# Kernel optimization log

Measured on AMD Instinct MI355X. Metric: run time of the kernel, lower is better.

Reference implementation:

```python
import jax, jax.numpy as jnp
import numpy as np

B, T = 64, 512
V, F, H = 30000, 256, 256
K = 32          # type_num
PAD, START, END = 0, 30, 31


def make_transition():
    # replicate the exact init order of the torch code
    t = jnp.zeros((K, K), jnp.float32)
    t = t.at[:, START].set(-10000.0)
    t = t.at[END, :].set(-10000.0)
    t = t.at[:, PAD].set(-10000.0)
    t = t.at[PAD, PAD].set(0.0)
    t = t.at[PAD, :END].set(0.0)
    return t


def setup_inputs() -> dict:
    key = jax.random.key(0)
    ks = jax.random.split(key, 12)
    x = jax.random.randint(ks[0], (B, T), 0, V, dtype=jnp.int32)
    tags = jax.random.randint(ks[1], (B, T), 1, START, dtype=jnp.int32)  # real tags, no pad/start/end
    lengths = jax.random.randint(ks[2], (B,), T // 2, T + 1, dtype=jnp.int32)
    mask = (jnp.arange(T, dtype=jnp.int32)[None, :] < lengths[:, None]).astype(jnp.int32)
    s = 0.05
    emb = jax.random.normal(ks[3], (V, F), jnp.float32) * (2.0 / (V + F)) ** 0.5 * 10  # xavier-ish
    w_ih_f = jax.random.normal(ks[4], (4 * H, F), jnp.float32) * s
    w_hh_f = jax.random.normal(ks[5], (4 * H, H), jnp.float32) * s
    b_f = jax.random.normal(ks[6], (4 * H,), jnp.float32) * s  # = b_ih + b_hh (they only ever sum)
    w_ih_b = jax.random.normal(ks[7], (4 * H, F), jnp.float32) * s
    w_hh_b = jax.random.normal(ks[8], (4 * H, H), jnp.float32) * s
    b_b = jax.random.normal(ks[9], (4 * H,), jnp.float32) * s
    w_fc = jax.random.normal(ks[10], (K, 2 * H), jnp.float32) * s
    b_fc = jax.random.normal(ks[11], (K,), jnp.float32) * s
    transition = make_transition()
    return dict(x=x, tags=tags, mask=mask, emb=emb,
                w_ih_f=w_ih_f, w_hh_f=w_hh_f, b_f=b_f,
                w_ih_b=w_ih_b, w_hh_b=w_hh_b, b_b=b_b,
                w_fc=w_fc, b_fc=b_fc, transition=transition)


def _lstm_scan(gx, w_hh):
    # gx: [T, B, 4H] precomputed input gates; PyTorch gate order i, f, g, o
    h0 = jnp.zeros((gx.shape[1], w_hh.shape[1]), gx.dtype)

    def step(carry, g):
        h, c = carry
        z = g + h @ w_hh.T
        i, f, gg, o = jnp.split(z, 4, axis=-1)
        c = jax.nn.sigmoid(f) * c + jax.nn.sigmoid(i) * jnp.tanh(gg)
        h = jax.nn.sigmoid(o) * jnp.tanh(c)
        return (h, c), h

    _, hs = jax.lax.scan(step, (h0, h0), gx)
    return hs  # [T, B, H]


def _crf_loss(scores, tags, mask, transition):
    # scores: [B, T, K], tags/mask: [B, T]
    maskf = mask.astype(scores.dtype)
    b_idx = jnp.arange(scores.shape[0])

    # ---- true path score ----
    first = transition[START, tags[:, 0]] + scores[b_idx, 0, tags[:, 0]]
    tag_sc = jnp.take_along_axis(scores, tags[..., None].astype(jnp.int32), axis=2)[..., 0]  # [B,T]
    tran_sc = transition[tags[:, :-1], tags[:, 1:]]  # [B,T-1]
    body = jnp.sum((tran_sc + tag_sc[:, 1:]) * maskf[:, 1:], axis=1)
    last_idx = jnp.sum(mask, axis=1) - 1
    last_tag = jnp.take_along_axis(tags, last_idx[:, None], axis=1)[:, 0]
    true_prob = first + body + transition[last_tag, END]

    # ---- partition (forward algorithm) via scan ----
    alpha0 = transition[START][None, :] + scores[:, 0]  # [B,K]

    def step(alpha, inp):
        sc, m = inp  # sc: [B,K], m: [B]
        new = jax.nn.logsumexp(alpha[:, :, None] + transition[None, :, :] + sc[:, None, :], axis=1)
        alpha = jnp.where(m[:, None] > 0, new, alpha)
        return alpha, None

    alpha, _ = jax.lax.scan(step, alpha0,
                            (scores.transpose(1, 0, 2)[1:], mask.T[1:]))
    total_prob = jax.nn.logsumexp(alpha + transition[:, END][None, :], axis=1)
    return -jnp.sum(true_prob - total_prob)


def reference(x, tags, mask, emb, w_ih_f, w_hh_f, b_f, w_ih_b, w_hh_b, b_b, w_fc, b_fc, transition):
    e = emb[x]                       # [B,T,F] embedding lookup (dropout = identity, eval mode)
    xt = e.transpose(1, 0, 2)        # [T,B,F]
    # forward direction
    h_f = _lstm_scan(xt @ w_ih_f.T + b_f, w_hh_f)           # [T,B,H]
    # backward direction: reverse time, scan, reverse back
    h_b = _lstm_scan((xt @ w_ih_b.T + b_b)[::-1], w_hh_b)[::-1]
    h = jnp.concatenate([h_f, h_b], axis=-1).transpose(1, 0, 2)  # [B,T,2H]
    scores = h @ w_fc.T + b_fc       # [B,T,K]
    return _crf_loss(scores, tags, mask, transition)
```

## Files before the change

### kernel.cpp

```cpp
#include <hip/hip_runtime.h>

typedef __attribute__((ext_vector_type(8))) short short8;
typedef __attribute__((ext_vector_type(4))) float floatx4;
typedef __attribute__((ext_vector_type(8))) int int8v;

__device__ __forceinline__ float bf2f(unsigned short u) {
    union { unsigned int i; float f; } c; c.i = ((unsigned int)u) << 16; return c.f;
}
__device__ __forceinline__ unsigned short f2bf(float f) {
    union { float f; unsigned int i; } c; c.f = f;
    unsigned int u = c.i;
    return (unsigned short)((u + 0x7FFFu + ((u >> 16) & 1u)) >> 16);
}
__device__ __forceinline__ unsigned short f2bf_rz(float f) {
    union { float f; unsigned int i; } c; c.f = f;
    return (unsigned short)(c.i >> 16);
}
__device__ __forceinline__ float sigm(float x) {
    return __builtin_amdgcn_rcpf(1.f + __expf(-x));
}
__device__ __forceinline__ float tanh_(float x) {
    return 1.f - 2.f * __builtin_amdgcn_rcpf(1.f + __expf(2.f * x));
}

__device__ __forceinline__ void glds16(const void* g, void* l) {
    __builtin_amdgcn_global_load_lds((const __attribute__((address_space(1))) unsigned int*)g,
                                     (__attribute__((address_space(3))) unsigned int*)l, 16, 0, 0);
}

__global__ void k_prep(const int* __restrict__ x, const float* __restrict__ emb,
                       unsigned short* __restrict__ et,
                       const float* __restrict__ wihf, const float* __restrict__ wihb,
                       const float* __restrict__ wfc, unsigned short* __restrict__ wbf,
                       const float* __restrict__ whhf, const float* __restrict__ whhb,
                       unsigned char* __restrict__ w8) {
    const int bid = blockIdx.x;
    if (bid < 4096) {
        int id = bid * 256 + threadIdx.x;
        int m = id >> 5, fi = (id & 31) << 3;
        int b = m & 63, t = m >> 6;
        int v = x[b * 512 + t];
        const float4* s = (const float4*)(emb + ((size_t)v << 8) + fi);
        float4 a = s[0], q = s[1];
        uint4 o;
        o.x = (unsigned)f2bf(a.x) | ((unsigned)f2bf(a.y) << 16);
        o.y = (unsigned)f2bf(a.z) | ((unsigned)f2bf(a.w) << 16);
        o.z = (unsigned)f2bf(q.x) | ((unsigned)f2bf(q.y) << 16);
        o.w = (unsigned)f2bf(q.z) | ((unsigned)f2bf(q.w) << 16);
        *(uint4*)(et + ((size_t)m << 8) + fi) = o;
    } else if (bid < 6176) {
        int i = (bid - 4096) * 256 + threadIdx.x;
        if (i >= 532480) return;
        float v;
        if (i < 262144) v = wihf[i];
        else if (i < 524288) v = wihb[i - 262144];
        else v = wfc[i - 524288];
        wbf[i] = f2bf(v);
    } else {
        int i = (bid - 6176) * 256 + threadIdx.x;
        if (i >= 262144) return;
        int e = i * 2;
        float a = (e < 262144) ? whhf[e] : whhb[e - 262144];
        float b = (e + 1 < 262144) ? whhf[e + 1] : whhb[e + 1 - 262144];
        int p = __builtin_amdgcn_cvt_pk_fp8_f32(a, b, 0, false);
        *(unsigned short*)(w8 + e) = (unsigned short)(p & 0xffff);
    }
}

__global__ __launch_bounds__(256, 2) void k_gx(const unsigned short* __restrict__ et,
                                               const unsigned short* __restrict__ wcat,
                                               const float* __restrict__ bfv, const float* __restrict__ bbv,
                                               unsigned short* __restrict__ gx) {
    __shared__ unsigned short As[4096];
    __shared__ unsigned short Bs[4096];
    const int tid = threadIdx.x;
    const int w = tid >> 6, l = tid & 63, quad = l >> 4, col = l & 15;
    const size_t m0 = (size_t)blockIdx.x * 128, n0 = (size_t)blockIdx.y * 128;
    floatx4 C[4][4];
    #pragma unroll
    for (int i = 0; i < 4; ++i)
        #pragma unroll
        for (int j = 0; j < 4; ++j) C[i][j] = (floatx4){0.f, 0.f, 0.f, 0.f};
    const int srow = tid >> 2, scol = (tid & 3) * 16;
    for (int it = 0; it < 8; ++it) {
        const char* ga = (const char*)et + (m0 + srow) * 512 + it * 64 + scol;
        const char* gb = (const char*)wcat + (n0 + srow) * 512 + it * 64 + scol;
        glds16(ga,             (char*)As + w * 1024);
        glds16(ga + 64 * 512,  (char*)As + 4096 + w * 1024);
        glds16(gb,             (char*)Bs + w * 1024);
        glds16(gb + 64 * 512,  (char*)Bs + 4096 + w * 1024);
        __syncthreads();
        short8 Af[4], Bf[4];
        #pragma unroll
        for (int i = 0; i < 4; ++i) {
            Af[i] = *(const short8*)(As + (((w & 1) * 64 + i * 16 + col) * 32 + quad * 8));
            Bf[i] = *(const short8*)(Bs + (((w >> 1) * 64 + i * 16 + col) * 32 + quad * 8));
        }
        #pragma unroll
        for (int i = 0; i < 4; ++i)
            #pragma unroll
            for (int j = 0; j < 4; ++j)
                C[i][j] = __builtin_amdgcn_mfma_f32_16x16x32_bf16(Af[i], Bf[j], C[i][j], 0, 0, 0);
        __syncthreads();
    }
    const int mw = (w & 1) * 64, nw = (w >> 1) * 64;
    #pragma unroll
    for (int j = 0; j < 4; ++j) {
        int n = (int)n0 + nw + j * 16 + col;
        float bias = (n < 1024) ? bfv[n] : bbv[n - 1024];
        size_t dbase = (size_t)(n >> 10) * 33554432 + (size_t)(n & 1023);
        #pragma unroll
        for (int i = 0; i < 4; ++i)
            #pragma unroll
            for (int r = 0; r < 4; ++r) {
                size_t m = m0 + mw + i * 16 + quad * 4 + r;
                gx[dbase + m * 1024] = f2bf(C[i][j][r] + bias);
            }
    }
}

__global__ __launch_bounds__(512, 2) void k_lstm(const unsigned char* __restrict__ w8_all,
                                                 const unsigned short* __restrict__ gx_all,
                                                 unsigned short* __restrict__ hcat) {
    const int d = blockIdx.x >> 5, bg = blockIdx.x & 31;
    const int tid = threadIdx.x, w = tid >> 6, l = tid & 63, quad = l >> 4, col = l & 15;
    const unsigned char* W = w8_all + (size_t)d * 262144;
    const unsigned short* G = gx_all + (size_t)d * 33554432;
    __shared__ __align__(16) unsigned char hld[2][2][288];

    int8v Wb[4][2][2];
    #pragma unroll
    for (int g = 0; g < 4; ++g)
        #pragma unroll
        for (int nt = 0; nt < 2; ++nt)
            #pragma unroll
            for (int kt = 0; kt < 2; ++kt)
                Wb[g][nt][kt] = *(const int8v*)(W + (size_t)(256 * g + 32 * w + 16 * nt + col) * 256
                                                + kt * 128 + quad * 32);
    for (int i = tid; i < 288; i += 512) ((unsigned int*)hld)[i] = 0;

    const int b = l >> 5, u = 32 * w + (l & 31);
    const int bglob = 2 * bg + b;
    const int nts = quad & 1;
    const int hsel = (l >> 3) & 1;
    float cst = 0.f;
    const long gstep = d ? -65536 : 65536;
    const long hstep = d ? -32768 : 32768;
    const unsigned short* gp = G + ((size_t)((d ? 511 : 0) * 64 + bglob) * 1024 + u);
    unsigned short* hp = hcat + ((size_t)((d ? 511 : 0) * 64 + bglob) * 512 + d * 256 + u);
    unsigned short gq0 = gp[0], gq1 = gp[256], gq2 = gp[512], gq3 = gp[768];
    gp += gstep;
    __syncthreads();

    #pragma clang loop unroll(disable)
    for (int step = 0; step < 512; ++step) {
        const int cur = step & 1;
        int8v Af[2];
        #pragma unroll
        for (int kt = 0; kt < 2; ++kt)
            Af[kt] = *(const int8v*)(&hld[cur][hsel][kt * 128 + quad * 32]);
        float z[4];
        #pragma unroll
        for (int g = 0; g < 4; ++g) {
            floatx4 c0 = (floatx4){0.f, 0.f, 0.f, 0.f};
            floatx4 c1 = (floatx4){0.f, 0.f, 0.f, 0.f};
            #pragma unroll
            for (int kt = 0; kt < 2; ++kt) {
                c0 = __builtin_amdgcn_mfma_scale_f32_16x16x128_f8f6f4(
                    Af[kt], Wb[g][0][kt], c0, 0, 0, 0, 0x7f7f7f7f, 0, 0x7f7f7f7f);
                c1 = __builtin_amdgcn_mfma_scale_f32_16x16x128_f8f6f4(
                    Af[kt], Wb[g][1][kt], c1, 0, 0, 0, 0x7f7f7f7f, 0, 0x7f7f7f7f);
            }
            z[g] = nts ? c1[0] : c0[0];
        }
        float vi = z[0] + bf2f(gq0);
        float vf = z[1] + bf2f(gq1);
        float vg = z[2] + bf2f(gq2);
        float vo = z[3] + bf2f(gq3);
        gq0 = gp[0]; gq1 = gp[256]; gq2 = gp[512]; gq3 = gp[768];
        gp += gstep;
        float cc = sigm(vf) * cst + sigm(vi) * tanh_(vg);
        cst = cc;
        float hf = sigm(vo) * tanh_(cc);
        *hp = f2bf_rz(hf);
        hp += hstep;
        int pk = __builtin_amdgcn_cvt_pk_fp8_f32(hf, hf, 0, false);
        hld[cur ^ 1][b][u] = (unsigned char)(pk & 0xff);
        __builtin_amdgcn_sched_barrier(0);
        asm volatile("s_waitcnt lgkmcnt(0)");
        __builtin_amdgcn_sched_barrier(0);
        __builtin_amdgcn_s_barrier();
        __builtin_amdgcn_sched_barrier(0);
    }
}

__global__ __launch_bounds__(256, 4) void k_scores(const unsigned short* __restrict__ hcat,
                                                   const unsigned short* __restrict__ wfc,
                                                   const float* __restrict__ bfc,
                                                   float* __restrict__ sc) {
    const int tid = threadIdx.x, w = tid >> 6, l = tid & 63, quad = l >> 4, col = l & 15;
    const int m0 = blockIdx.x * 64 + w * 16;
    floatx4 C0 = (floatx4){0.f, 0.f, 0.f, 0.f}, C1 = C0;
    #pragma unroll
    for (int kt = 0; kt < 16; ++kt) {
        short8 A  = *(const short8*)(hcat + (size_t)(m0 + col) * 512 + kt * 32 + quad * 8);
        short8 B0 = *(const short8*)(wfc + (size_t)col * 512 + kt * 32 + quad * 8);
        short8 B1 = *(const short8*)(wfc + (size_t)(16 + col) * 512 + kt * 32 + quad * 8);
        C0 = __builtin_amdgcn_mfma_f32_16x16x32_bf16(A, B0, C0, 0, 0, 0);
        C1 = __builtin_amdgcn_mfma_f32_16x16x32_bf16(A, B1, C1, 0, 0, 0);
    }
    float b0 = bfc[col], b1 = bfc[16 + col];
    #pragma unroll
    for (int r = 0; r < 4; ++r) {
        int m = m0 + quad * 4 + r;
        sc[(size_t)m * 32 + col] = C0[r] + b0;
        sc[(size_t)m * 32 + 16 + col] = C1[r] + b1;
    }
}

__global__ __launch_bounds__(1024, 1) void k_crf(const float* __restrict__ sc, const int* __restrict__ tags,
                                                 const int* __restrict__ mask, const float* __restrict__ tr,
                                                 float* __restrict__ out) {
    __shared__ float Tm[32][33];
    __shared__ float al[2][32];
    __shared__ float trueb;
    const int b = blockIdx.x, tid = threadIdx.x;
    { int i = tid >> 5, j = tid & 31; Tm[i][j] = tr[tid]; }
    __syncthreads();
    if (tid < 64) {
        float acc = 0.f; int cnt = 0;
        for (int t = tid; t < 512; t += 64) cnt += mask[b * 512 + t];
        for (int t = tid + 1; t < 512; t += 64) {
            if (mask[b * 512 + t]) {
                int tg = tags[b * 512 + t], tp = tags[b * 512 + t - 1];
                acc += Tm[tp][tg] + sc[((size_t)t * 64 + b) * 32 + tg];
            }
        }
        #pragma unroll
        for (int m = 1; m < 64; m <<= 1) { acc += __shfl_xor(acc, m); cnt += __shfl_xor(cnt, m); }
        if (tid == 0) {
            int tg0 = tags[b * 512];
            float first = Tm[30][tg0] + sc[(size_t)b * 32 + tg0];
            int lt = tags[b * 512 + cnt - 1];
            trueb = first + acc + Tm[lt][31];
        }
    }
    if (tid < 32) al[0][tid] = Tm[30][tid] + sc[(size_t)b * 32 + tid];
    __syncthreads();
    const int j = tid >> 5, i = tid & 31;
    int cur = 0;
    float scn = sc[((size_t)64 + b) * 32 + j];
    int mkn = mask[b * 512 + 1];
    #pragma clang loop unroll(disable)
    for (int t = 1; t < 512; ++t) {
        float v = al[cur][i] + Tm[i][j];
        float mx = v;
        #pragma unroll
        for (int m = 1; m < 32; m <<= 1) mx = fmaxf(mx, __shfl_xor(mx, m));
        float e = __expf(v - mx);
        #pragma unroll
        for (int m = 1; m < 32; m <<= 1) e += __shfl_xor(e, m);
        float nv = mx + __logf(e) + scn;
        int mk = mkn;
        int tn = t < 511 ? t + 1 : 511;
        scn = sc[((size_t)tn * 64 + b) * 32 + j];
        mkn = mask[b * 512 + tn];
        if (i == 0) al[cur ^ 1][j] = mk ? nv : al[cur][j];
        __syncthreads();
        cur ^= 1;
    }
    if (tid < 32) {
        float v = al[cur][tid] + Tm[tid][31];
        float mx = v;
        #pragma unroll
        for (int m = 1; m < 32; m <<= 1) mx = fmaxf(mx, __shfl_xor(mx, m));
        float e = __expf(v - mx);
        #pragma unroll
        for (int m = 1; m < 32; m <<= 1) e += __shfl_xor(e, m);
        if (tid == 0) atomicAdd(out, mx + __logf(e) - trueb);
    }
}

extern "C" void kernel_launch(void* const* d_in, const int* in_sizes, int n_in,
                              void* d_out, int out_size, void* d_ws, size_t ws_size,
                              hipStream_t stream) {
    const int* x      = (const int*)d_in[0];
    const int* tags   = (const int*)d_in[1];
    const int* mask   = (const int*)d_in[2];
    const float* emb  = (const float*)d_in[3];
    const float* wihf = (const float*)d_in[4];
    const float* whhf = (const float*)d_in[5];
    const float* bf_  = (const float*)d_in[6];
    const float* wihb = (const float*)d_in[7];
    const float* whhb = (const float*)d_in[8];
    const float* bb_  = (const float*)d_in[9];
    const float* wfc  = (const float*)d_in[10];
    const float* bfc  = (const float*)d_in[11];
    const float* tr   = (const float*)d_in[12];

    char* ws = (char*)d_ws;
    unsigned short* et   = (unsigned short*)(ws);
    unsigned short* wbf  = (unsigned short*)(ws + 16777216);
    unsigned char*  w8   = (unsigned char*)(ws + 17842176);
    unsigned short* gx   = (unsigned short*)(ws + 18366464);
    unsigned short* hcat = (unsigned short*)(ws + 152584192);
    float* sc            = (float*)(ws + 186138624);

    hipMemsetAsync(d_out, 0, sizeof(float), stream);
    k_prep<<<7200, 256, 0, stream>>>(x, emb, et, wihf, wihb, wfc, wbf, whhf, whhb, w8);
    dim3 g2(256, 16);
    k_gx<<<g2, 256, 0, stream>>>(et, wbf, bf_, bb_, gx);
    k_lstm<<<64, 512, 0, stream>>>(w8, gx, hcat);
    k_scores<<<512, 256, 0, stream>>>(hcat, wbf + 524288, bfc, sc);
    k_crf<<<64, 1024, 0, stream>>>(sc, tags, mask, tr, (float*)d_out);
}
```

Measured before the change: 909.7 us.

## Interleave gate columns so each LSTM thread loads its four gates in one 8-byte read

```diff
diff --git a/kernel.cpp b/kernel.cpp
--- a/kernel.cpp
+++ b/kernel.cpp
@@ -6,6 +6,9 @@
 
 __device__ __forceinline__ float bf2f(unsigned short u) {
     union { unsigned int i; float f; } c; c.i = ((unsigned int)u) << 16; return c.f;
+}
+__device__ __forceinline__ float asf(unsigned int u) {
+    union { unsigned int i; float f; } c; c.i = u; return c.f;
 }
 __device__ __forceinline__ unsigned short f2bf(float f) {
     union { float f; unsigned int i; } c; c.f = f;
@@ -52,9 +55,13 @@
         int i = (bid - 4096) * 256 + threadIdx.x;
         if (i >= 532480) return;
         float v;
-        if (i < 262144) v = wihf[i];
-        else if (i < 524288) v = wihb[i - 262144];
-        else v = wfc[i - 524288];
+        if (i < 524288) {
+            int r = (i >> 8) & 1023, c = i & 255;
+            int src = (256 * (r & 3) + (r >> 2)) * 256 + c;
+            v = (i < 262144) ? wihf[src] : wihb[src];
+        } else {
+            v = wfc[i - 524288];
+        }
         wbf[i] = f2bf(v);
     } else {
         int i = (bid - 6176) * 256 + threadIdx.x;
@@ -107,8 +114,10 @@
     #pragma unroll
     for (int j = 0; j < 4; ++j) {
         int n = (int)n0 + nw + j * 16 + col;
-        float bias = (n < 1024) ? bfv[n] : bbv[n - 1024];
-        size_t dbase = (size_t)(n >> 10) * 33554432 + (size_t)(n & 1023);
+        int nl = n & 1023;
+        int bidx = ((nl >> 2) & 255) + 256 * (nl & 3);
+        float bias = (n < 1024) ? bfv[bidx] : bbv[bidx];
+        size_t dbase = (size_t)(n >> 10) * 33554432 + (size_t)nl;
         #pragma unroll
         for (int i = 0; i < 4; ++i)
             #pragma unroll
@@ -146,9 +155,9 @@
     float cst = 0.f;
     const long gstep = d ? -65536 : 65536;
     const long hstep = d ? -32768 : 32768;
-    const unsigned short* gp = G + ((size_t)((d ? 511 : 0) * 64 + bglob) * 1024 + u);
+    const unsigned short* gp = G + ((size_t)((d ? 511 : 0) * 64 + bglob) * 1024 + u * 4);
     unsigned short* hp = hcat + ((size_t)((d ? 511 : 0) * 64 + bglob) * 512 + d * 256 + u);
-    unsigned short gq0 = gp[0], gq1 = gp[256], gq2 = gp[512], gq3 = gp[768];
+    uint2 gq = *(const uint2*)gp;
     gp += gstep;
     __syncthreads();
 
@@ -173,11 +182,11 @@
             }
             z[g] = nts ? c1[0] : c0[0];
         }
-        float vi = z[0] + bf2f(gq0);
-        float vf = z[1] + bf2f(gq1);
-        float vg = z[2] + bf2f(gq2);
-        float vo = z[3] + bf2f(gq3);
-        gq0 = gp[0]; gq1 = gp[256]; gq2 = gp[512]; gq3 = gp[768];
+        float vi = z[0] + asf(gq.x << 16);
+        float vf = z[1] + asf(gq.x & 0xffff0000u);
+        float vg = z[2] + asf(gq.y << 16);
+        float vo = z[3] + asf(gq.y & 0xffff0000u);
+        gq = *(const uint2*)gp;
         gp += gstep;
         float cc = sigm(vf) * cst + sigm(vi) * tanh_(vg);
         cst = cc;
```

Measured after the change: 887.5 us. 2.4% less time.
